# Performance work log

Measured on AMD Instinct MI355X. Metric: run time of the kernel, lower is better.

## Reference

```python
import jax
import jax.numpy as jnp
from jax import lax
import numpy as np

B, CIN, COUT, RANK, K, H, W = 16, 256, 256, 64, 3, 112, 112
PAD = 1


def setup_inputs() -> dict:
    key = jax.random.key(0)
    k1, k2, k3, k4, k5 = jax.random.split(key, 5)
    x = jax.random.normal(k1, (B, CIN, H, W), dtype=jnp.float32)
    # head: `rank` stacked 1x1 conv weights, each [COUT, CIN]
    w_head = jax.random.normal(k2, (RANK, COUT, CIN), dtype=jnp.float32) * 0.05
    # body: Conv2d(COUT -> RANK, kernel (K,1)), OIHW layout
    w_body = jax.random.normal(k3, (RANK, COUT, K, 1), dtype=jnp.float32) * 0.05
    # tail: Conv2d(RANK -> COUT, kernel (1,K)), OIHW layout, with bias
    w_tail = jax.random.normal(k4, (COUT, RANK, 1, K), dtype=jnp.float32) * 0.05
    b_tail = jax.random.normal(k5, (COUT,), dtype=jnp.float32) * 0.05
    return {"x": x, "w_head": w_head, "w_body": w_body, "w_tail": w_tail, "b_tail": b_tail}


_DN = lax.conv_dimension_numbers((B, CIN, H, W), (COUT, CIN, 1, 1), ("NCHW", "OIHW", "NCHW"))


def reference(x, w_head, w_body, w_tail, b_tail):
    # Sum of rank 1x1 convs over the same input == one 1x1 conv with summed
    # weights (conv is linear in the weight) — same math, one pass.
    w_sum = w_head.sum(axis=0)                      # [COUT, CIN]
    y = jnp.einsum("bihw,oi->bohw", x, w_sum)       # [B, COUT, H, W]
    # body: (K,1) conv, stride (1,1), padding (PAD, 0)
    y = lax.conv_general_dilated(y, w_body, window_strides=(1, 1),
                                 padding=((PAD, PAD), (0, 0)),
                                 dimension_numbers=_DN)  # [B, RANK, H, W]
    # tail: (1,K) conv, stride (1,1), padding (0, PAD), plus bias
    y = lax.conv_general_dilated(y, w_tail, window_strides=(1, 1),
                                 padding=((0, 0), (PAD, PAD)),
                                 dimension_numbers=_DN)  # [B, COUT, H, W]
    return y + b_tail[None, :, None, None]
```

## Files before the change

kernel.cpp:

```cpp
#include <hip/hip_runtime.h>
#include <stdint.h>

#define CIN 256
#define COUT 256
#define RANK 64
#define H_ 112
#define W_ 112
#define HW_ (112*112)

typedef short bf16x8 __attribute__((ext_vector_type(8)));
typedef float f32x4 __attribute__((ext_vector_type(4)));

__device__ __forceinline__ unsigned rne2(float a, float b){
  unsigned ua = __builtin_bit_cast(unsigned, a);
  unsigned ub = __builtin_bit_cast(unsigned, b);
  ua += 0x7FFFu + ((ua >> 16) & 1u);
  ub += 0x7FFFu + ((ub >> 16) & 1u);
  return (ua >> 16) | (ub & 0xFFFF0000u);
}
__device__ __forceinline__ unsigned short rne1(float a){
  unsigned ua = __builtin_bit_cast(unsigned, a);
  ua += 0x7FFFu + ((ua >> 16) & 1u);
  return (unsigned short)(ua >> 16);
}

__global__ __launch_bounds__(256) void k_pre1(const float* __restrict__ x,
                                              unsigned short* __restrict__ xt,
                                              const float* __restrict__ wh,
                                              float* __restrict__ wsum,
                                              int base_b, int nb){
  __shared__ float ldsf[64*120];
  const int tid = threadIdx.x;
  if (blockIdx.x >= (unsigned)(nb*114)){
    int o = blockIdx.x - nb*114;
    float s = 0.f;
    for (int k = 0; k < RANK; ++k) s += wh[(k*COUT + o)*CIN + tid];
    wsum[o*CIN + tid] = s;
    return;
  }
  const int lb = blockIdx.x / 114, hh = blockIdx.x % 114;
  const int bb = base_b + lb;
  const int h = hh - 1;
  unsigned short* dst = xt + ((size_t)(lb*114 + hh))*28672;

  if (h < 0 || h >= H_){
    uint4 z = {0,0,0,0};
    #pragma unroll
    for (int j = 0; j < 14; ++j)
      *(uint4*)(dst + (tid + 256*j)*8) = z;
    return;
  }

  for (int i0p = 0; i0p < 4; ++i0p){
    int c = tid / 28, wq = tid % 28;
    #pragma unroll
    for (int j = 0; j < 7; ++j){
      const float4 v = *(const float4*)(x + ((size_t)(bb*CIN + i0p*64 + c))*HW_ + h*W_ + wq*4);
      *(float4*)&ldsf[c*120 + wq*4] = v;
      wq += 4; c += 9; if (wq >= 28){ wq -= 28; c += 1; }
    }
    __syncthreads();
    for (int ck = tid; ck < 896; ck += 256){
      int g8 = ck / 112, w = ck % 112;
      const float* src = &ldsf[(g8*8)*120 + w];
      uint4 st;
      st.x = rne2(src[0],     src[120]);
      st.y = rne2(src[240],   src[360]);
      st.z = rne2(src[480],   src[600]);
      st.w = rne2(src[720],   src[840]);
      *(uint4*)(dst + (size_t)(i0p*896 + ck)*8) = st;
    }
    __syncthreads();
  }
}

__global__ __launch_bounds__(256) void k_pre2(const float* __restrict__ wb,
                                              const float* __restrict__ wsum,
                                              unsigned short* __restrict__ weff,
                                              const float* __restrict__ wt,
                                              unsigned short* __restrict__ wtp){
  const int tid = threadIdx.x;
  if (blockIdx.x < 192){
    int bid = blockIdx.x;
    int dh = bid >> 6, r = bid & 63;
    float s = 0.f;
    for (int o = 0; o < COUT; ++o)
      s += wb[(r*COUT + o)*3 + dh] * wsum[o*CIN + tid];
    weff[bid*CIN + tid] = rne1(s);
  } else {
    int o = blockIdx.x - 192;
    if (tid < 192){
      int dw = tid >> 6, r = tid & 63;
      wtp[o*192 + tid] = rne1(wt[(o*RANK + r)*3 + dw]);
    }
  }
}

__global__ __launch_bounds__(256,2) void k_fused(const unsigned short* __restrict__ xt,
                                                 const unsigned short* __restrict__ weff,
                                                 const unsigned short* __restrict__ wtp,
                                                 const float* __restrict__ bias,
                                                 float* __restrict__ out,
                                                 int base_b){
  __shared__ alignas(16) unsigned short lds[28672];
  const int tid  = threadIdx.x;
  const int wid  = tid >> 6, lane = tid & 63, g = lane >> 4, l15 = lane & 15;
  const int lb   = blockIdx.x / 56, hb = blockIdx.x % 56;
  const int bb   = base_b + lb;
  const int h0   = hb*2;
  const int hloc = wid >> 1, rhalf = wid & 1;

  f32x4 acc[2][7];
  #pragma unroll
  for (int a = 0; a < 2; ++a)
    #pragma unroll
    for (int b = 0; b < 7; ++b) acc[a][b] = (f32x4){0.f,0.f,0.f,0.f};

  const unsigned short* rowbase = xt + ((size_t)(lb*114 + h0 + wid)*8)*3584;

  auto stage = [&](unsigned short* dstbuf, int i0){
    const unsigned short* src = rowbase + (size_t)i0*3584 + lane*8;
    unsigned short* dstb = dstbuf + wid*3584;
    #pragma unroll
    for (int k = 0; k < 7; ++k)
      __builtin_amdgcn_global_load_lds(
        (const __attribute__((address_space(1))) void*)(src + k*512),
        (__attribute__((address_space(3))) void*)(dstb + k*512), 16, 0, 0);
  };

  auto compute = [&](const unsigned short* buf, int i0){
    #pragma unroll
    for (int dh = 0; dh < 3; ++dh){
      const int row = hloc + dh;
      const unsigned short* ab = weff + (size_t)(dh*64 + rhalf*32 + l15)*CIN + i0*32 + g*8;
      bf16x8 af0 = *(const bf16x8*)(ab);
      bf16x8 af1 = *(const bf16x8*)(ab + 16*CIN);
      const unsigned short* qb = buf + row*3584 + g*896 + l15*8;
      #pragma unroll
      for (int wt = 0; wt < 7; ++wt){
        bf16x8 bfv = *(const bf16x8*)(qb + wt*128);
        acc[0][wt] = __builtin_amdgcn_mfma_f32_16x16x32_bf16(af0, bfv, acc[0][wt], 0, 0, 0);
        acc[1][wt] = __builtin_amdgcn_mfma_f32_16x16x32_bf16(af1, bfv, acc[1][wt], 0, 0, 0);
      }
    }
  };

  unsigned short* cur = lds;
  unsigned short* nxt = lds + 14336;
  stage(cur, 0);
  __syncthreads();
  for (int t = 0; t < 8; ++t){
    if (t < 7) stage(nxt, t+1);
    compute(cur, t);
    __syncthreads();
    unsigned short* tmp = cur; cur = nxt; nxt = tmp;
  }

  unsigned short* y2b = lds;
  if (tid < 32){
    int hh = tid >> 4, wsel = (tid >> 3) & 1, rq = tid & 7;
    *(uint4*)(y2b + hh*8208 + (wsel ? 113 : 0)*72 + rq*8) = (uint4){0,0,0,0};
  }
  #pragma unroll
  for (int wt = 0; wt < 7; ++wt){
    #pragma unroll
    for (int rt = 0; rt < 2; ++rt){
      unsigned lo = rne2(acc[rt][wt][0], acc[rt][wt][1]);
      unsigned hi = rne2(acc[rt][wt][2], acc[rt][wt][3]);
      uint2 st; st.x = lo; st.y = hi;
      *(uint2*)(y2b + hloc*8208 + (wt*16 + l15 + 1)*72 + rhalf*32 + rt*16 + g*4) = st;
    }
  }
  __syncthreads();

  const int h = h0 + hloc;
  #pragma unroll
  for (int opass = 0; opass < 2; ++opass){
    const int obase = rhalf*128 + opass*64;
    f32x4 a2[4][7];
    #pragma unroll
    for (int a = 0; a < 4; ++a)
      #pragma unroll
      for (int b = 0; b < 7; ++b) a2[a][b] = (f32x4){0.f,0.f,0.f,0.f};

    #pragma unroll
    for (int s = 0; s < 6; ++s){
      bf16x8 af[4];
      const unsigned short* ab = wtp + (size_t)(obase + l15)*192 + s*32 + g*8;
      #pragma unroll
      for (int rt = 0; rt < 4; ++rt)
        af[rt] = *(const bf16x8*)(ab + rt*16*192);
      const unsigned short* qb = y2b + hloc*8208 + (l15 + (s >> 1))*72 + (s & 1)*32 + g*8;
      #pragma unroll
      for (int wt = 0; wt < 7; ++wt){
        bf16x8 bv = *(const bf16x8*)(qb + wt*16*72);
        #pragma unroll
        for (int rt = 0; rt < 4; ++rt)
          a2[rt][wt] = __builtin_amdgcn_mfma_f32_16x16x32_bf16(af[rt], bv, a2[rt][wt], 0, 0, 0);
      }
    }

    float* ob = out + ((size_t)(bb*COUT) + obase)*HW_ + h*W_;
    #pragma unroll
    for (int rt = 0; rt < 4; ++rt){
      #pragma unroll
      for (int ii = 0; ii < 4; ++ii){
        float bvv = bias[obase + rt*16 + g*4 + ii];
        #pragma unroll
        for (int wt = 0; wt < 7; ++wt)
          ob[(size_t)(rt*16 + g*4 + ii)*HW_ + wt*16 + l15] = a2[rt][wt][ii] + bvv;
      }
    }
  }
}

extern "C" void kernel_launch(void* const* d_in, const int* in_sizes, int n_in,
                              void* d_out, int out_size, void* d_ws, size_t ws_size,
                              hipStream_t stream) {
  const float* x      = (const float*)d_in[0];
  const float* w_head = (const float*)d_in[1];
  const float* w_body = (const float*)d_in[2];
  const float* w_tail = (const float*)d_in[3];
  const float* b_tail = (const float*)d_in[4];
  float* out = (float*)d_out;
  char* ws = (char*)d_ws;

  float*          wsum = (float*)ws;
  unsigned short* weff = (unsigned short*)(ws + 262144);
  unsigned short* wtp  = (unsigned short*)(ws + 360448);
  unsigned short* xt   = (unsigned short*)(ws + 458752);

  const size_t XT_ROW_BYTES = 57344;
  const size_t XT_PER_B     = 114 * XT_ROW_BYTES;
  size_t avail = (ws_size > 458752) ? ws_size - 458752 : 0;
  int chunk_b = (int)(avail / XT_PER_B);
  if (chunk_b > 16) chunk_b = 16;
  if (chunk_b < 1)  chunk_b = 1;
  int nchunks = (16 + chunk_b - 1) / chunk_b;

  int base = 0;
  for (int c = 0; c < nchunks; ++c){
    int remaining = 16 - base;
    int nb = (remaining + (nchunks - c) - 1) / (nchunks - c);
    k_pre1<<<nb*114 + (c == 0 ? 256 : 0), 256, 0, stream>>>(x, xt, w_head, wsum, base, nb);
    if (c == 0)
      k_pre2<<<448, 256, 0, stream>>>(w_body, wsum, weff, w_tail, wtp);
    k_fused<<<nb*56, 256, 0, stream>>>(xt, weff, wtp, b_tail, out, base);
    base += nb;
  }
}
```

Baseline: 181.6 us.

## Enlarge fused tile to four output rows with swizzled LDS and split pre1 blocks

The fused kernel now processes four output rows per block instead of two. Each wave owns one row and all 64 rank channels, so the staged input rows (6 instead of 4) are reused across more outputs. Staging moves from async global_load_lds double buffering to register-staged single-buffer loads. The intermediate LDS tile uses an XOR swizzle to cut bank conflicts. k_pre1 is split four ways per row to expose more parallelism and drop the inner sync loop. The change risks higher register pressure, less overlap between load and compute, and half as many fused blocks for occupancy.

```diff
diff --git a/kernel.cpp b/kernel.cpp
--- a/kernel.cpp
+++ b/kernel.cpp
@@ -10,6 +10,8 @@
 
 typedef short bf16x8 __attribute__((ext_vector_type(8)));
 typedef float f32x4 __attribute__((ext_vector_type(4)));
+
+#define SWZ(a) ((a) ^ ((((a) >> 7) & 7) << 4))
 
 __device__ __forceinline__ unsigned rne2(float a, float b){
   unsigned ua = __builtin_bit_cast(unsigned, a);
@@ -31,27 +33,28 @@
                                               int base_b, int nb){
   __shared__ float ldsf[64*120];
   const int tid = threadIdx.x;
-  if (blockIdx.x >= (unsigned)(nb*114)){
-    int o = blockIdx.x - nb*114;
+  if (blockIdx.x >= (unsigned)(nb*456)){
+    int o = blockIdx.x - nb*456;
     float s = 0.f;
     for (int k = 0; k < RANK; ++k) s += wh[(k*COUT + o)*CIN + tid];
     wsum[o*CIN + tid] = s;
     return;
   }
-  const int lb = blockIdx.x / 114, hh = blockIdx.x % 114;
-  const int bb = base_b + lb;
-  const int h = hh - 1;
-  unsigned short* dst = xt + ((size_t)(lb*114 + hh))*28672;
+  const int lb  = blockIdx.x / 456;
+  const int rem = blockIdx.x % 456;
+  const int hh  = rem >> 2, i0p = rem & 3;
+  const int bb  = base_b + lb;
+  const int h   = hh - 1;
+  unsigned short* dst = xt + ((size_t)(lb*114 + hh))*28672 + (size_t)i0p*7168;
 
   if (h < 0 || h >= H_){
     uint4 z = {0,0,0,0};
-    #pragma unroll
-    for (int j = 0; j < 14; ++j)
-      *(uint4*)(dst + (tid + 256*j)*8) = z;
+    for (int ck = tid; ck < 896; ck += 256)
+      *(uint4*)(dst + ck*8) = z;
     return;
   }
 
-  for (int i0p = 0; i0p < 4; ++i0p){
+  {
     int c = tid / 28, wq = tid % 28;
     #pragma unroll
     for (int j = 0; j < 7; ++j){
@@ -59,18 +62,17 @@
       *(float4*)&ldsf[c*120 + wq*4] = v;
       wq += 4; c += 9; if (wq >= 28){ wq -= 28; c += 1; }
     }
-    __syncthreads();
-    for (int ck = tid; ck < 896; ck += 256){
-      int g8 = ck / 112, w = ck % 112;
-      const float* src = &ldsf[(g8*8)*120 + w];
-      uint4 st;
-      st.x = rne2(src[0],     src[120]);
-      st.y = rne2(src[240],   src[360]);
-      st.z = rne2(src[480],   src[600]);
-      st.w = rne2(src[720],   src[840]);
-      *(uint4*)(dst + (size_t)(i0p*896 + ck)*8) = st;
-    }
-    __syncthreads();
+  }
+  __syncthreads();
+  for (int ck = tid; ck < 896; ck += 256){
+    int g8 = ck / 112, w = ck % 112;
+    const float* src = &ldsf[(g8*8)*120 + w];
+    uint4 st;
+    st.x = rne2(src[0],     src[120]);
+    st.y = rne2(src[240],   src[360]);
+    st.z = rne2(src[480],   src[600]);
+    st.w = rne2(src[720],   src[840]);
+    *(uint4*)(dst + ck*8) = st;
   }
 }
 
@@ -102,81 +104,91 @@
                                                  const float* __restrict__ bias,
                                                  float* __restrict__ out,
                                                  int base_b){
-  __shared__ alignas(16) unsigned short lds[28672];
+  __shared__ alignas(16) unsigned short lds[29184];
   const int tid  = threadIdx.x;
   const int wid  = tid >> 6, lane = tid & 63, g = lane >> 4, l15 = lane & 15;
-  const int lb   = blockIdx.x / 56, hb = blockIdx.x % 56;
+  const int lb   = blockIdx.x / 28, hb = blockIdx.x % 28;
   const int bb   = base_b + lb;
-  const int h0   = hb*2;
-  const int hloc = wid >> 1, rhalf = wid & 1;
-
-  f32x4 acc[2][7];
+  const int h0   = hb*4;
+
+  f32x4 acc[4][7];
   #pragma unroll
-  for (int a = 0; a < 2; ++a)
+  for (int a = 0; a < 4; ++a)
     #pragma unroll
     for (int b = 0; b < 7; ++b) acc[a][b] = (f32x4){0.f,0.f,0.f,0.f};
 
-  const unsigned short* rowbase = xt + ((size_t)(lb*114 + h0 + wid)*8)*3584;
-
-  auto stage = [&](unsigned short* dstbuf, int i0){
-    const unsigned short* src = rowbase + (size_t)i0*3584 + lane*8;
-    unsigned short* dstb = dstbuf + wid*3584;
-    #pragma unroll
-    for (int k = 0; k < 7; ++k)
-      __builtin_amdgcn_global_load_lds(
-        (const __attribute__((address_space(1))) void*)(src + k*512),
-        (__attribute__((address_space(3))) void*)(dstb + k*512), 16, 0, 0);
+  uint4 sv[11];
+  auto load_step = [&](int i0){
+    #pragma unroll
+    for (int j = 0; j < 11; ++j){
+      int cid = tid + 256*j;
+      if (cid < 2688){
+        int row = cid / 448, off = cid % 448;
+        sv[j] = *(const uint4*)(xt + ((size_t)((lb*114 + h0 + row)*8 + i0))*3584 + off*8);
+      }
+    }
   };
-
-  auto compute = [&](const unsigned short* buf, int i0){
+  auto write_step = [&](){
+    #pragma unroll
+    for (int j = 0; j < 11; ++j){
+      int cid = tid + 256*j;
+      if (cid < 2688){
+        int row = cid / 448, off = cid % 448;
+        *(uint4*)(lds + row*3584 + off*8) = sv[j];
+      }
+    }
+  };
+  auto compute = [&](int i0){
     #pragma unroll
     for (int dh = 0; dh < 3; ++dh){
-      const int row = hloc + dh;
-      const unsigned short* ab = weff + (size_t)(dh*64 + rhalf*32 + l15)*CIN + i0*32 + g*8;
-      bf16x8 af0 = *(const bf16x8*)(ab);
-      bf16x8 af1 = *(const bf16x8*)(ab + 16*CIN);
-      const unsigned short* qb = buf + row*3584 + g*896 + l15*8;
+      bf16x8 af[4];
+      const unsigned short* ab = weff + (size_t)(dh*64 + l15)*CIN + i0*32 + g*8;
+      #pragma unroll
+      for (int rt = 0; rt < 4; ++rt)
+        af[rt] = *(const bf16x8*)(ab + rt*16*CIN);
+      const unsigned short* qb = lds + (wid + dh)*3584 + g*896 + l15*8;
       #pragma unroll
       for (int wt = 0; wt < 7; ++wt){
         bf16x8 bfv = *(const bf16x8*)(qb + wt*128);
-        acc[0][wt] = __builtin_amdgcn_mfma_f32_16x16x32_bf16(af0, bfv, acc[0][wt], 0, 0, 0);
-        acc[1][wt] = __builtin_amdgcn_mfma_f32_16x16x32_bf16(af1, bfv, acc[1][wt], 0, 0, 0);
+        #pragma unroll
+        for (int rt = 0; rt < 4; ++rt)
+          acc[rt][wt] = __builtin_amdgcn_mfma_f32_16x16x32_bf16(af[rt], bfv, acc[rt][wt], 0, 0, 0);
       }
     }
   };
 
-  unsigned short* cur = lds;
-  unsigned short* nxt = lds + 14336;
-  stage(cur, 0);
+  load_step(0);
+  for (int t = 0; t < 8; ++t){
+    __syncthreads();
+    write_step();
+    __syncthreads();
+    if (t < 7) load_step(t+1);
+    compute(t);
+  }
   __syncthreads();
-  for (int t = 0; t < 8; ++t){
-    if (t < 7) stage(nxt, t+1);
-    compute(cur, t);
-    __syncthreads();
-    unsigned short* tmp = cur; cur = nxt; nxt = tmp;
-  }
-
-  unsigned short* y2b = lds;
-  if (tid < 32){
-    int hh = tid >> 4, wsel = (tid >> 3) & 1, rq = tid & 7;
-    *(uint4*)(y2b + hh*8208 + (wsel ? 113 : 0)*72 + rq*8) = (uint4){0,0,0,0};
+
+  unsigned char* y2b = (unsigned char*)lds;
+  if (tid < 64){
+    int hz = tid >> 4, wsel = (tid >> 3) & 1, q = tid & 7;
+    unsigned a = (unsigned)(hz*14592 + (wsel ? 113 : 0)*128 + q*16);
+    *(uint4*)(y2b + SWZ(a)) = (uint4){0,0,0,0};
   }
   #pragma unroll
   for (int wt = 0; wt < 7; ++wt){
     #pragma unroll
-    for (int rt = 0; rt < 2; ++rt){
+    for (int rt = 0; rt < 4; ++rt){
       unsigned lo = rne2(acc[rt][wt][0], acc[rt][wt][1]);
       unsigned hi = rne2(acc[rt][wt][2], acc[rt][wt][3]);
       uint2 st; st.x = lo; st.y = hi;
-      *(uint2*)(y2b + hloc*8208 + (wt*16 + l15 + 1)*72 + rhalf*32 + rt*16 + g*4) = st;
+      unsigned a = (unsigned)(wid*14592 + (wt*16 + l15 + 1)*128 + rt*32 + g*8);
+      *(uint2*)(y2b + SWZ(a)) = st;
     }
   }
   __syncthreads();
 
-  const int h = h0 + hloc;
   #pragma unroll
-  for (int opass = 0; opass < 2; ++opass){
-    const int obase = rhalf*128 + opass*64;
+  for (int opass = 0; opass < 4; ++opass){
+    const int obase = opass*64;
     f32x4 a2[4][7];
     #pragma unroll
     for (int a = 0; a < 4; ++a)
@@ -190,17 +202,17 @@
       #pragma unroll
       for (int rt = 0; rt < 4; ++rt)
         af[rt] = *(const bf16x8*)(ab + rt*16*192);
-      const unsigned short* qb = y2b + hloc*8208 + (l15 + (s >> 1))*72 + (s & 1)*32 + g*8;
       #pragma unroll
       for (int wt = 0; wt < 7; ++wt){
-        bf16x8 bv = *(const bf16x8*)(qb + wt*16*72);
+        unsigned a = (unsigned)(wid*14592 + (wt*16 + l15 + (s>>1))*128 + (s&1)*64 + g*16);
+        bf16x8 bv = *(const bf16x8*)(y2b + SWZ(a));
         #pragma unroll
         for (int rt = 0; rt < 4; ++rt)
           a2[rt][wt] = __builtin_amdgcn_mfma_f32_16x16x32_bf16(af[rt], bv, a2[rt][wt], 0, 0, 0);
       }
     }
 
-    float* ob = out + ((size_t)(bb*COUT) + obase)*HW_ + h*W_;
+    float* ob = out + ((size_t)(bb*COUT) + obase)*HW_ + (h0 + wid)*W_;
     #pragma unroll
     for (int rt = 0; rt < 4; ++rt){
       #pragma unroll
@@ -230,8 +242,7 @@
   unsigned short* wtp  = (unsigned short*)(ws + 360448);
   unsigned short* xt   = (unsigned short*)(ws + 458752);
 
-  const size_t XT_ROW_BYTES = 57344;
-  const size_t XT_PER_B     = 114 * XT_ROW_BYTES;
+  const size_t XT_PER_B = (size_t)114 * 57344;
   size_t avail = (ws_size > 458752) ? ws_size - 458752 : 0;
   int chunk_b = (int)(avail / XT_PER_B);
   if (chunk_b > 16) chunk_b = 16;
@@ -242,10 +253,10 @@
   for (int c = 0; c < nchunks; ++c){
     int remaining = 16 - base;
     int nb = (remaining + (nchunks - c) - 1) / (nchunks - c);
-    k_pre1<<<nb*114 + (c == 0 ? 256 : 0), 256, 0, stream>>>(x, xt, w_head, wsum, base, nb);
+    k_pre1<<<nb*456 + (c == 0 ? 256 : 0), 256, 0, stream>>>(x, xt, w_head, wsum, base, nb);
     if (c == 0)
       k_pre2<<<448, 256, 0, stream>>>(w_body, wsum, weff, w_tail, wtp);
-    k_fused<<<nb*56, 256, 0, stream>>>(xt, weff, wtp, b_tail, out, base);
+    k_fused<<<nb*28, 256, 0, stream>>>(xt, weff, wtp, b_tail, out, base);
     base += nb;
   }
 }
```

New measurement: 247.2 us. +36.2%, slower.

## Stage output tiles through LDS for coalesced stores and remap blocks across XCDs

Applied to the files above, without the earlier changes.

The epilogue now writes each wave's 16x112 output tile into a per-wave LDS scratch region, then issues row-contiguous float2 global stores, replacing the previous scattered 4-byte stores along the output-channel stride. Block IDs are also remapped so that consecutive logical tiles are grouped per XCD (orig&7 chooses the group), aiming for better L2 locality on the shared rows. LDS use grows, which may reduce occupancy, and the extra LDS round trip adds latency. The remap assumes nb*56 is divisible by 8.

```diff
diff --git a/kernel.cpp b/kernel.cpp
--- a/kernel.cpp
+++ b/kernel.cpp
@@ -101,11 +101,13 @@
                                                  const unsigned short* __restrict__ wtp,
                                                  const float* __restrict__ bias,
                                                  float* __restrict__ out,
-                                                 int base_b){
-  __shared__ alignas(16) unsigned short lds[28672];
+                                                 int base_b, unsigned cpx){
+  __shared__ alignas(16) unsigned short lds[31264];
   const int tid  = threadIdx.x;
   const int wid  = tid >> 6, lane = tid & 63, g = lane >> 4, l15 = lane & 15;
-  const int lb   = blockIdx.x / 56, hb = blockIdx.x % 56;
+  const unsigned orig = blockIdx.x;
+  const unsigned wg   = (orig & 7u)*cpx + (orig >> 3);
+  const int lb   = wg / 56, hb = wg % 56;
   const int bb   = base_b + lb;
   const int h0   = hb*2;
   const int hloc = wid >> 1, rhalf = wid & 1;
@@ -174,6 +176,7 @@
   __syncthreads();
 
   const int h = h0 + hloc;
+  float* tb = (float*)(lds + 16416) + wid*1856;
   #pragma unroll
   for (int opass = 0; opass < 2; ++opass){
     const int obase = rhalf*128 + opass*64;
@@ -200,15 +203,30 @@
       }
     }
 
-    float* ob = out + ((size_t)(bb*COUT) + obase)*HW_ + h*W_;
-    #pragma unroll
-    for (int rt = 0; rt < 4; ++rt){
+    #pragma unroll
+    for (int rt = 0; rt < 4; ++rt)
       #pragma unroll
       for (int ii = 0; ii < 4; ++ii){
         float bvv = bias[obase + rt*16 + g*4 + ii];
         #pragma unroll
-        for (int wt = 0; wt < 7; ++wt)
-          ob[(size_t)(rt*16 + g*4 + ii)*HW_ + wt*16 + l15] = a2[rt][wt][ii] + bvv;
+        for (int wt = 0; wt < 7; ++wt) a2[rt][wt][ii] += bvv;
+      }
+
+    #pragma unroll
+    for (int rt = 0; rt < 4; ++rt){
+      #pragma unroll
+      for (int wt = 0; wt < 7; ++wt)
+        #pragma unroll
+        for (int ii = 0; ii < 4; ++ii)
+          tb[(g*4 + ii)*116 + wt*16 + l15] = a2[rt][wt][ii];
+      if (lane < 56){
+        const int w2 = 2*lane;
+        float* ob = out + ((size_t)(bb*COUT + obase + rt*16))*HW_ + h*W_ + w2;
+        #pragma unroll
+        for (int o16 = 0; o16 < 16; ++o16){
+          float2 v = *(float2*)&tb[o16*116 + w2];
+          *(float2*)(ob + (size_t)o16*HW_) = v;
+        }
       }
     }
   }
@@ -230,8 +248,7 @@
   unsigned short* wtp  = (unsigned short*)(ws + 360448);
   unsigned short* xt   = (unsigned short*)(ws + 458752);
 
-  const size_t XT_ROW_BYTES = 57344;
-  const size_t XT_PER_B     = 114 * XT_ROW_BYTES;
+  const size_t XT_PER_B = (size_t)114 * 57344;
   size_t avail = (ws_size > 458752) ? ws_size - 458752 : 0;
   int chunk_b = (int)(avail / XT_PER_B);
   if (chunk_b > 16) chunk_b = 16;
@@ -245,7 +262,7 @@
     k_pre1<<<nb*114 + (c == 0 ? 256 : 0), 256, 0, stream>>>(x, xt, w_head, wsum, base, nb);
     if (c == 0)
       k_pre2<<<448, 256, 0, stream>>>(w_body, wsum, weff, w_tail, wtp);
-    k_fused<<<nb*56, 256, 0, stream>>>(xt, weff, wtp, b_tail, out, base);
+    k_fused<<<nb*56, 256, 0, stream>>>(xt, weff, wtp, b_tail, out, base, (unsigned)(nb*7));
     base += nb;
   }
 }
```

Measured after the change: 186.6 us. 2.7% more time.

## Hand-pipeline fused kernel main loop with explicit waitcnt, barriers and MFMA priority

Applied to the files above, without the earlier changes.

Reworks the fused kernel's K-loop. The A-fragment weight loads for the next step are now issued before the async global-to-LDS stage. __syncthreads is replaced by explicit s_waitcnt vmcnt counts plus s_barrier so that only the current buffer's loads are waited on. LDS B-fragments are batched ahead of each MFMA group, and MFMA sections are wrapped in s_setprio. The aim is to overlap global loads with MFMA and cut synchronisation stalls, at the cost of relying on hand-counted vmcnt values and more registers.

```diff
diff --git a/kernel.cpp b/kernel.cpp
--- a/kernel.cpp
+++ b/kernel.cpp
@@ -117,6 +117,7 @@
     for (int b = 0; b < 7; ++b) acc[a][b] = (f32x4){0.f,0.f,0.f,0.f};
 
   const unsigned short* rowbase = xt + ((size_t)(lb*114 + h0 + wid)*8)*3584;
+  const unsigned short* wbase   = weff + (size_t)(rhalf*32 + l15)*CIN + g*8;
 
   auto stage = [&](unsigned short* dstbuf, int i0){
     const unsigned short* src = rowbase + (size_t)i0*3584 + lane*8;
@@ -128,31 +129,47 @@
         (__attribute__((address_space(3))) void*)(dstb + k*512), 16, 0, 0);
   };
 
-  auto compute = [&](const unsigned short* buf, int i0){
+  bf16x8 af[3][2];
+  auto loadA = [&](int i0){
+    #pragma unroll
+    for (int dh = 0; dh < 3; ++dh)
+      #pragma unroll
+      for (int rt = 0; rt < 2; ++rt)
+        af[dh][rt] = *(const bf16x8*)(wbase + (size_t)(dh*64 + rt*16)*CIN + i0*32);
+  };
+
+  auto compute = [&](const unsigned short* buf){
     #pragma unroll
     for (int dh = 0; dh < 3; ++dh){
-      const int row = hloc + dh;
-      const unsigned short* ab = weff + (size_t)(dh*64 + rhalf*32 + l15)*CIN + i0*32 + g*8;
-      bf16x8 af0 = *(const bf16x8*)(ab);
-      bf16x8 af1 = *(const bf16x8*)(ab + 16*CIN);
-      const unsigned short* qb = buf + row*3584 + g*896 + l15*8;
+      const unsigned short* qb = buf + (hloc + dh)*3584 + g*896 + l15*8;
+      bf16x8 bfv[7];
+      #pragma unroll
+      for (int wt = 0; wt < 7; ++wt) bfv[wt] = *(const bf16x8*)(qb + wt*128);
+      __builtin_amdgcn_s_setprio(1);
       #pragma unroll
       for (int wt = 0; wt < 7; ++wt){
-        bf16x8 bfv = *(const bf16x8*)(qb + wt*128);
-        acc[0][wt] = __builtin_amdgcn_mfma_f32_16x16x32_bf16(af0, bfv, acc[0][wt], 0, 0, 0);
-        acc[1][wt] = __builtin_amdgcn_mfma_f32_16x16x32_bf16(af1, bfv, acc[1][wt], 0, 0, 0);
+        acc[0][wt] = __builtin_amdgcn_mfma_f32_16x16x32_bf16(af[dh][0], bfv[wt], acc[0][wt], 0, 0, 0);
+        acc[1][wt] = __builtin_amdgcn_mfma_f32_16x16x32_bf16(af[dh][1], bfv[wt], acc[1][wt], 0, 0, 0);
       }
+      __builtin_amdgcn_s_setprio(0);
     }
   };
 
   unsigned short* cur = lds;
   unsigned short* nxt = lds + 14336;
   stage(cur, 0);
-  __syncthreads();
   for (int t = 0; t < 8; ++t){
+    loadA(t);
+    __builtin_amdgcn_sched_barrier(0);
     if (t < 7) stage(nxt, t+1);
-    compute(cur, t);
-    __syncthreads();
+    __builtin_amdgcn_sched_barrier(0);
+    if (t < 7) asm volatile("s_waitcnt vmcnt(13)" ::: "memory");
+    else       asm volatile("s_waitcnt vmcnt(6)"  ::: "memory");
+    __builtin_amdgcn_s_barrier();
+    __builtin_amdgcn_sched_barrier(0);
+    compute(cur);
+    __builtin_amdgcn_sched_barrier(0);
+    __builtin_amdgcn_s_barrier();
     unsigned short* tmp = cur; cur = nxt; nxt = tmp;
   }
 
@@ -185,19 +202,22 @@
 
     #pragma unroll
     for (int s = 0; s < 6; ++s){
-      bf16x8 af[4];
+      bf16x8 afc[4];
       const unsigned short* ab = wtp + (size_t)(obase + l15)*192 + s*32 + g*8;
       #pragma unroll
       for (int rt = 0; rt < 4; ++rt)
-        af[rt] = *(const bf16x8*)(ab + rt*16*192);
+        afc[rt] = *(const bf16x8*)(ab + rt*16*192);
       const unsigned short* qb = y2b + hloc*8208 + (l15 + (s >> 1))*72 + (s & 1)*32 + g*8;
-      #pragma unroll
-      for (int wt = 0; wt < 7; ++wt){
-        bf16x8 bv = *(const bf16x8*)(qb + wt*16*72);
+      bf16x8 bv[7];
+      #pragma unroll
+      for (int wt = 0; wt < 7; ++wt) bv[wt] = *(const bf16x8*)(qb + wt*16*72);
+      __builtin_amdgcn_s_setprio(1);
+      #pragma unroll
+      for (int wt = 0; wt < 7; ++wt)
         #pragma unroll
         for (int rt = 0; rt < 4; ++rt)
-          a2[rt][wt] = __builtin_amdgcn_mfma_f32_16x16x32_bf16(af[rt], bv, a2[rt][wt], 0, 0, 0);
-      }
+          a2[rt][wt] = __builtin_amdgcn_mfma_f32_16x16x32_bf16(afc[rt], bv[wt], a2[rt][wt], 0, 0, 0);
+      __builtin_amdgcn_s_setprio(0);
     }
 
     float* ob = out + ((size_t)(bb*COUT) + obase)*HW_ + h*W_;
@@ -230,8 +250,7 @@
   unsigned short* wtp  = (unsigned short*)(ws + 360448);
   unsigned short* xt   = (unsigned short*)(ws + 458752);
 
-  const size_t XT_ROW_BYTES = 57344;
-  const size_t XT_PER_B     = 114 * XT_ROW_BYTES;
+  const size_t XT_PER_B = (size_t)114 * 57344;
   size_t avail = (ws_size > 458752) ? ws_size - 458752 : 0;
   int chunk_b = (int)(avail / XT_PER_B);
   if (chunk_b > 16) chunk_b = 16;
```

After: 183.7 us. Within noise of the previous version (+1.2%).
